# Kernel optimization log

Hardware: AMD Instinct MI355X
Metric: run time of the kernel (lower is better)

The kernel has to match this reference:

```python
import jax, jax.numpy as jnp
import numpy as np

N_HEADS = 8
N_DIM = 512
ATTN_DIM = N_DIM // N_HEADS
SOFT_TEMPERATURE = 1.0
TEMPERATURE = ATTN_DIM ** 0.5 / SOFT_TEMPERATURE


def sparsemax(z):
    # sparsemax along last axis: euclidean projection onto the simplex
    n = z.shape[-1]
    z_sorted = -jnp.sort(-z, axis=-1)                      # descending
    cs = jnp.cumsum(z_sorted, axis=-1)
    k = jnp.arange(1, n + 1, dtype=z.dtype)
    support = 1.0 + k * z_sorted > cs                      # bool
    k_sel = jnp.sum(support, axis=-1, keepdims=True)       # support size >= 1
    cs_sel = jnp.take_along_axis(cs, k_sel - 1, axis=-1)
    tau = (cs_sel - 1.0) / k_sel.astype(z.dtype)
    return jnp.maximum(z - tau, 0.0)


def setup_inputs() -> dict:
    key = jax.random.key(0)
    ks = jax.random.split(key, 9)
    bs, L, d = 8, 1024, N_DIM
    s = 1.0 / np.sqrt(d)
    return {
        "h_q": jax.random.normal(ks[0], (bs, L, d), jnp.float32),
        "h_k": jax.random.normal(ks[1], (bs, L, d), jnp.float32),
        "h_v": jax.random.normal(ks[2], (bs, L, d), jnp.float32),
        "Wq": jax.random.normal(ks[3], (d, d), jnp.float32) * s,
        "Wk": jax.random.normal(ks[4], (d, d), jnp.float32) * s,
        "Wv": jax.random.normal(ks[5], (d, d), jnp.float32) * s,
        "bv": jax.random.normal(ks[6], (d,), jnp.float32) * s,
        "Wf": jax.random.normal(ks[7], (d, d), jnp.float32) * s,
        "bf": jax.random.normal(ks[8], (d,), jnp.float32) * s,
    }


def reference(h_q, h_k, h_v, Wq, Wk, Wv, bv, Wf, bf):
    bs, Lq, _ = h_q.shape
    Lk = h_k.shape[1]
    H, D = N_HEADS, ATTN_DIM
    q = (h_q @ Wq.T).reshape(bs, Lq, H, D).transpose(0, 2, 1, 3)   # bhqd
    k = (h_k @ Wk.T).reshape(bs, Lk, H, D).transpose(0, 2, 1, 3)   # bhkd
    v = (h_v @ Wv.T + bv).reshape(bs, Lk, H, D).transpose(0, 2, 1, 3)
    alpha = jnp.einsum('bhqd,bhkd->bhqk', q / TEMPERATURE, k)
    alpha = sparsemax(alpha)
    res = jnp.einsum('bhqk,bhkd->bhqd', alpha, v)
    res = res.transpose(0, 2, 1, 3).reshape(bs, Lq, H * D)
    return res @ Wf.T + bf
```

## Files before the change

kernel.cpp:

```cpp
#include <hip/hip_runtime.h>
#include <hip/hip_bf16.h>
#include <cstdint>
#include <cstddef>

#define BS 8
#define SEQ 1024
#define DMODEL 512
#define NHEADS 8
#define DHEAD 64
#define QBLK 16
#define PPAD 1032

typedef float f32x4 __attribute__((ext_vector_type(4)));
typedef short bf16x8 __attribute__((ext_vector_type(8)));

static __device__ __forceinline__ unsigned short f2bf(float v) {
    __hip_bfloat16 hb = __float2bfloat16(v);
    return *reinterpret_cast<unsigned short*>(&hb);
}

struct CvtJob { const float* s; unsigned short* d; int n4; };

__global__ __launch_bounds__(256) void cvt_many(
    CvtJob j0, CvtJob j1, CvtJob j2, CvtJob j3, CvtJob j4, CvtJob j5, CvtJob j6)
{
    CvtJob j;
    switch (blockIdx.y) {
        case 0: j = j0; break; case 1: j = j1; break; case 2: j = j2; break;
        case 3: j = j3; break; case 4: j = j4; break; case 5: j = j5; break;
        default: j = j6; break;
    }
    for (int i = blockIdx.x * 256 + threadIdx.x; i < j.n4; i += gridDim.x * 256) {
        const float4 f = ((const float4*)j.s)[i];
        uint2 u;
        u.x = (unsigned)f2bf(f.x) | ((unsigned)f2bf(f.y) << 16);
        u.y = (unsigned)f2bf(f.z) | ((unsigned)f2bf(f.w) << 16);
        ((uint2*)j.d)[i] = u;
    }
}

struct GArgs { const unsigned short* A; const unsigned short* W;
               const float* bias; void* C; float scale; int mode; };

__global__ __launch_bounds__(256) void gemm_mfma(GArgs g0, GArgs g1, GArgs g2) {
    __shared__ __align__(16) unsigned short As[64 * 64];
    __shared__ __align__(16) unsigned short Bs[128 * 64];

    const GArgs g = (blockIdx.z == 0) ? g0 : ((blockIdx.z == 1) ? g1 : g2);
    const int tid = threadIdx.x;
    const int w = tid >> 6, l = tid & 63, lr = l & 15, lg = l >> 4;
    const int bm = blockIdx.y * 64, bn = blockIdx.x * 128;
    const int mrow = (w & 1) * 32, ncol = (w >> 1) * 64;

    f32x4 acc[2][4];
#pragma unroll
    for (int mt = 0; mt < 2; ++mt)
#pragma unroll
        for (int nt = 0; nt < 4; ++nt) acc[mt][nt] = (f32x4)0.f;

    for (int k0 = 0; k0 < DMODEL; k0 += 64) {
#pragma unroll
        for (int i = 0; i < 2; ++i) {
            const int rbase = i * 32 + w * 8;
            const int r = rbase + (l >> 3);
            const unsigned short* src = g.A + (size_t)(bm + r) * DMODEL + k0
                                        + 8 * ((l & 7) ^ (r & 7));
            __builtin_amdgcn_global_load_lds((const unsigned int*)src,
                                             (unsigned int*)&As[rbase * 64], 16, 0, 0);
        }
#pragma unroll
        for (int i = 0; i < 4; ++i) {
            const int rbase = i * 32 + w * 8;
            const int r = rbase + (l >> 3);
            const unsigned short* src = g.W + (size_t)(bn + r) * DMODEL + k0
                                        + 8 * ((l & 7) ^ (r & 7));
            __builtin_amdgcn_global_load_lds((const unsigned int*)src,
                                             (unsigned int*)&Bs[rbase * 64], 16, 0, 0);
        }
        __syncthreads();
#pragma unroll
        for (int kk = 0; kk < 2; ++kk) {
            bf16x8 av[2], bv[4];
#pragma unroll
            for (int mt = 0; mt < 2; ++mt) {
                const int ra = mrow + mt * 16 + lr;
                av[mt] = *(const bf16x8*)&As[ra * 64 + 8 * ((kk * 4 + lg) ^ (ra & 7))];
            }
#pragma unroll
            for (int nt = 0; nt < 4; ++nt) {
                const int rb = ncol + nt * 16 + lr;
                bv[nt] = *(const bf16x8*)&Bs[rb * 64 + 8 * ((kk * 4 + lg) ^ (rb & 7))];
            }
#pragma unroll
            for (int mt = 0; mt < 2; ++mt)
#pragma unroll
                for (int nt = 0; nt < 4; ++nt)
                    acc[mt][nt] = __builtin_amdgcn_mfma_f32_16x16x32_bf16(
                        av[mt], bv[nt], acc[mt][nt], 0, 0, 0);
        }
        __syncthreads();
    }

    if (g.mode == 0) {
        float* C = (float*)g.C;
#pragma unroll
        for (int mt = 0; mt < 2; ++mt)
#pragma unroll
        for (int nt = 0; nt < 4; ++nt)
#pragma unroll
        for (int j = 0; j < 4; ++j) {
            const int r = bm + mrow + mt * 16 + lg * 4 + j;
            const int c = bn + ncol + nt * 16 + lr;
            C[(size_t)r * DMODEL + c] = acc[mt][nt][j] * g.scale
                                        + (g.bias ? g.bias[c] : 0.f);
        }
    } else if (g.mode == 1) {
        unsigned short* C = (unsigned short*)g.C;
#pragma unroll
        for (int mt = 0; mt < 2; ++mt)
#pragma unroll
        for (int nt = 0; nt < 4; ++nt)
#pragma unroll
        for (int j = 0; j < 4; ++j) {
            const int r = bm + mrow + mt * 16 + lg * 4 + j;
            const int c = bn + ncol + nt * 16 + lr;
            const float v = acc[mt][nt][j] * g.scale + (g.bias ? g.bias[c] : 0.f);
            const int b = r >> 10, ll = r & (SEQ - 1);
            const int h = c >> 6, dd = c & 63;
            C[((size_t)(b * NHEADS + h) * SEQ + ll) * DHEAD + dd] = f2bf(v);
        }
    } else {
        unsigned short* C = (unsigned short*)g.C;
#pragma unroll
        for (int mt = 0; mt < 2; ++mt)
#pragma unroll
        for (int nt = 0; nt < 4; ++nt) {
            const int c = bn + ncol + nt * 16 + lr;
            const int h = c >> 6, dd = c & 63;
            const int r0 = bm + mrow + mt * 16 + lg * 4;
            const int b = r0 >> 10, l0 = r0 & (SEQ - 1);
            unsigned short tmp[4];
#pragma unroll
            for (int j = 0; j < 4; ++j)
                tmp[j] = f2bf(acc[mt][nt][j] * g.scale + (g.bias ? g.bias[c] : 0.f));
            uint2 u;
            u.x = (unsigned)tmp[0] | ((unsigned)tmp[1] << 16);
            u.y = (unsigned)tmp[2] | ((unsigned)tmp[3] << 16);
            *(uint2*)&C[((size_t)(b * NHEADS + h) * DHEAD + dd) * SEQ + l0] = u;
        }
    }
}

__global__ __launch_bounds__(256, 4) void attn_mfma(
    const unsigned short* __restrict__ Q, const unsigned short* __restrict__ K,
    const unsigned short* __restrict__ Vt, unsigned short* __restrict__ R)
{
    __shared__ __align__(16) unsigned short P[QBLK][PPAD];
    __shared__ __align__(16) float clist[QBLK][68];
    __shared__ int cnt_s[QBLK];
    __shared__ __align__(16) float red_m[QBLK][4];
    __shared__ __align__(16) float red_s[2][QBLK][4];
    __shared__ __align__(16) float red_c[2][QBLK][4];

    const int tid = threadIdx.x;
    const int w = tid >> 6, l = tid & 63, lr = l & 15, lg = l >> 4;

    const int flat = blockIdx.x;
    const int nid = (flat & 7) * 512 + (flat >> 3);
    const int q0 = (nid & 63) * QBLK;
    const int h = (nid >> 6) & (NHEADS - 1);
    const int b = nid >> 9;

    const size_t base = (size_t)(b * NHEADS + h) * SEQ * DHEAD;
    const unsigned short* Qp = Q + base;
    const unsigned short* Kp = K + base;

    const int ks = w * 256;

    const bf16x8 aq0 = *(const bf16x8*)(Qp + (size_t)(q0 + lr) * DHEAD + lg * 8);
    const bf16x8 aq1 = *(const bf16x8*)(Qp + (size_t)(q0 + lr) * DHEAD + 32 + lg * 8);
#define KROW(T) (Kp + (size_t)(ks + (T) * 16 + lr) * DHEAD + lg * 8)
    bf16x8 ka0 = *(const bf16x8*)KROW(0), kb0 = *(const bf16x8*)(KROW(0) + 32);
    bf16x8 ka1 = *(const bf16x8*)KROW(1), kb1 = *(const bf16x8*)(KROW(1) + 32);
    bf16x8 ka2 = *(const bf16x8*)KROW(2), kb2 = *(const bf16x8*)(KROW(2) + 32);
    bf16x8 ka3 = *(const bf16x8*)KROW(3), kb3 = *(const bf16x8*)(KROW(3) + 32);
    f32x4 acc[16];
#pragma unroll
    for (int t = 0; t < 16; ++t) acc[t] = (f32x4)0.f;
#define QK_STEP(T, KA, KB)                                                     \
    {                                                                          \
        acc[T] = __builtin_amdgcn_mfma_f32_16x16x32_bf16(KA, aq0, acc[T], 0, 0, 0); \
        acc[T] = __builtin_amdgcn_mfma_f32_16x16x32_bf16(KB, aq1, acc[T], 0, 0, 0); \
        if ((T) + 4 < 16) {                                                    \
            KA = *(const bf16x8*)KROW((T) + 4);                                \
            KB = *(const bf16x8*)(KROW((T) + 4) + 32);                         \
        }                                                                      \
    }
#pragma unroll
    for (int t = 0; t < 16; t += 4) {
        QK_STEP(t + 0, ka0, kb0)
        QK_STEP(t + 1, ka1, kb1)
        QK_STEP(t + 2, ka2, kb2)
        QK_STEP(t + 3, ka3, kb3)
    }
#undef QK_STEP
#undef KROW

    f32x4 m4 = acc[0];
#pragma unroll
    for (int t = 1; t < 16; ++t) {
        m4[0] = fmaxf(m4[0], acc[t][0]); m4[1] = fmaxf(m4[1], acc[t][1]);
        m4[2] = fmaxf(m4[2], acc[t][2]); m4[3] = fmaxf(m4[3], acc[t][3]);
    }
    float m = fmaxf(fmaxf(m4[0], m4[1]), fmaxf(m4[2], m4[3]));
    m = fmaxf(m, __shfl_xor(m, 16));
    m = fmaxf(m, __shfl_xor(m, 32));
    if (lg == 0) red_m[lr][w] = m;

    for (int i = tid; i < QBLK * 68; i += 256) (&clist[0][0])[i] = -3.0e38f;
    if (tid < QBLK) cnt_s[tid] = 0;
    __syncthreads();

    const float4 rm4 = *(const float4*)red_m[lr];
    const float rmax = fmaxf(fmaxf(rm4.x, rm4.y), fmaxf(rm4.z, rm4.w));
    float tau = rmax - 1.0f;
    const float thr = tau;

#pragma unroll
    for (int t = 0; t < 16; ++t)
#pragma unroll
        for (int j = 0; j < 4; ++j) {
            const float z = acc[t][j];
            if (z > thr) {
                const int pos = atomicAdd(&cnt_s[lr], 1);
                if (pos < 64) clist[lr][pos] = z;
            }
        }
    __syncthreads();

    const bool anyfull = __any(cnt_s[lr] > 64);

    if (!anyfull) {
        const f32x4* clp = (const f32x4*)&clist[lr][lg * 16];
        const f32x4 cd0 = clp[0], cd1 = clp[1], cd2 = clp[2], cd3 = clp[3];
        for (int it = 0; it < 16; ++it) {
            float s = 0.f, c = 0.f;
#pragma unroll
            for (int i = 0; i < 4; ++i) {
                const float z0 = cd0[i], z1 = cd1[i], z2 = cd2[i], z3 = cd3[i];
                if (z0 > tau) { s += z0; c += 1.f; }
                if (z1 > tau) { s += z1; c += 1.f; }
                if (z2 > tau) { s += z2; c += 1.f; }
                if (z3 > tau) { s += z3; c += 1.f; }
            }
            s += __shfl_xor(s, 16); c += __shfl_xor(c, 16);
            s += __shfl_xor(s, 32); c += __shfl_xor(c, 32);
            const float tn = (s - 1.f) / c;
            float delta = tn - tau;
            tau = tn;
            delta = fmaxf(delta, __shfl_xor(delta, 1));
            delta = fmaxf(delta, __shfl_xor(delta, 2));
            delta = fmaxf(delta, __shfl_xor(delta, 4));
            delta = fmaxf(delta, __shfl_xor(delta, 8));
            if (delta < 1e-5f) break;
        }
    } else {
        for (int it = 0; it < 16; ++it) {
            const int bb = (it + 1) & 1;
            float s = 0.f, c = 0.f;
#pragma unroll
            for (int t = 0; t < 16; ++t)
#pragma unroll
                for (int j = 0; j < 4; ++j) {
                    const float z = acc[t][j];
                    if (z > tau) { s += z; c += 1.f; }
                }
            s += __shfl_xor(s, 16); c += __shfl_xor(c, 16);
            s += __shfl_xor(s, 32); c += __shfl_xor(c, 32);
            if (lg == 0) { red_s[bb][lr][w] = s; red_c[bb][lr][w] = c; }
            __syncthreads();
            const float4 s4 = *(const float4*)red_s[bb][lr];
            const float4 c4 = *(const float4*)red_c[bb][lr];
            const float st = (s4.x + s4.y) + (s4.z + s4.w);
            const float ct = (c4.x + c4.y) + (c4.z + c4.w);
            const float tn = (st - 1.f) / ct;
            float delta = tn - tau;
            tau = tn;
            delta = fmaxf(delta, __shfl_xor(delta, 1));
            delta = fmaxf(delta, __shfl_xor(delta, 2));
            delta = fmaxf(delta, __shfl_xor(delta, 4));
            delta = fmaxf(delta, __shfl_xor(delta, 8));
            if (delta < 1e-5f) break;
        }
    }

#pragma unroll
    for (int t = 0; t < 16; ++t)
#pragma unroll
        for (int jp = 0; jp < 2; ++jp) {
            const unsigned lo = f2bf(fmaxf(acc[t][2 * jp] - tau, 0.f));
            const unsigned hi = f2bf(fmaxf(acc[t][2 * jp + 1] - tau, 0.f));
            *(unsigned*)&P[lr][ks + t * 16 + lg * 4 + 2 * jp] = lo | (hi << 16);
        }
    __syncthreads();

    const int dcol = w * 16;
    const unsigned short* VtP = Vt + ((size_t)(b * NHEADS + h) * DHEAD + dcol + lr) * SEQ
                                + lg * 8;
    f32x4 o = (f32x4)0.f;
    bf16x8 vb0 = *(const bf16x8*)(VtP + 0 * 32);
    bf16x8 vb1 = *(const bf16x8*)(VtP + 1 * 32);
    bf16x8 vb2 = *(const bf16x8*)(VtP + 2 * 32);
    bf16x8 vb3 = *(const bf16x8*)(VtP + 3 * 32);
#define PV_STEP(KT, VREG)                                                      \
    {                                                                          \
        const bf16x8 pa = *(const bf16x8*)&P[lr][(KT) * 32 + lg * 8];          \
        __builtin_amdgcn_s_setprio(1);                                         \
        o = __builtin_amdgcn_mfma_f32_16x16x32_bf16(pa, VREG, o, 0, 0, 0);     \
        __builtin_amdgcn_s_setprio(0);                                         \
        if ((KT) + 4 < 32) VREG = *(const bf16x8*)(VtP + ((KT) + 4) * 32);     \
    }
    for (int kt = 0; kt < 32; kt += 4) {
        PV_STEP(kt + 0, vb0)
        PV_STEP(kt + 1, vb1)
        PV_STEP(kt + 2, vb2)
        PV_STEP(kt + 3, vb3)
    }
#undef PV_STEP

#pragma unroll
    for (int j = 0; j < 4; ++j)
        R[((size_t)b * SEQ + q0 + lg * 4 + j) * DMODEL + h * DHEAD + dcol + lr] =
            f2bf(o[j]);
}

extern "C" void kernel_launch(void* const* d_in, const int* in_sizes, int n_in,
                              void* d_out, int out_size, void* d_ws, size_t ws_size,
                              hipStream_t stream) {
    const float* h_q = (const float*)d_in[0];
    const float* h_k = (const float*)d_in[1];
    const float* h_v = (const float*)d_in[2];
    const float* Wq  = (const float*)d_in[3];
    const float* Wk  = (const float*)d_in[4];
    const float* Wv  = (const float*)d_in[5];
    const float* bv  = (const float*)d_in[6];
    const float* Wf  = (const float*)d_in[7];
    const float* bf  = (const float*)d_in[8];
    float* out = (float*)d_out;

    const size_t perT = (size_t)BS * SEQ * DMODEL;
    const size_t wN = (size_t)DMODEL * DMODEL;
    unsigned short* hq_b = (unsigned short*)d_ws;
    unsigned short* hk_b = hq_b + perT;
    unsigned short* hv_b = hk_b + perT;
    unsigned short* Qws  = hv_b + perT;
    unsigned short* Kws  = Qws + perT;
    unsigned short* Vtw  = Kws + perT;
    unsigned short* Rws  = Vtw + perT;
    unsigned short* Wqb  = Rws + perT;
    unsigned short* Wkb  = Wqb + wN;
    unsigned short* Wvb  = Wkb + wN;
    unsigned short* Wfb  = Wvb + wN;

    {
        CvtJob j0{h_q, hq_b, (int)(perT / 4)};
        CvtJob j1{h_k, hk_b, (int)(perT / 4)};
        CvtJob j2{h_v, hv_b, (int)(perT / 4)};
        CvtJob j3{Wq, Wqb, (int)(wN / 4)};
        CvtJob j4{Wk, Wkb, (int)(wN / 4)};
        CvtJob j5{Wv, Wvb, (int)(wN / 4)};
        CvtJob j6{Wf, Wfb, (int)(wN / 4)};
        cvt_many<<<dim3(512, 7), 256, 0, stream>>>(j0, j1, j2, j3, j4, j5, j6);
    }

    {
        GArgs gq{hq_b, Wqb, nullptr, Qws, 0.125f, 1};
        GArgs gk{hk_b, Wkb, nullptr, Kws, 1.0f, 1};
        GArgs gv{hv_b, Wvb, bv,      Vtw, 1.0f, 2};
        gemm_mfma<<<dim3(DMODEL / 128, BS * SEQ / 64, 3), 256, 0, stream>>>(gq, gk, gv);
    }

    attn_mfma<<<dim3(BS * NHEADS * (SEQ / QBLK)), 256, 0, stream>>>(Qws, Kws, Vtw, Rws);

    {
        GArgs gf{Rws, Wfb, bf, out, 1.0f, 0};
        gemm_mfma<<<dim3(DMODEL / 128, BS * SEQ / 64, 1), 256, 0, stream>>>(gf, gf, gf);
    }
}
```

Before: 192.8 us.

## Compute sparse PV product by gathering V rows for sparsemax support only

Alongside each candidate score, the kernel now stores that score's key index. In the common path where every row's support fits in 64 candidates, the full P matrix write and the dense PV MFMA loop are skipped. Instead each thread gathers the selected V rows from a new row-major V copy and accumulates weighted sums directly. The V projection GEMM writes both transposed and row-major layouts, which adds global writes and workspace. The s_setprio hints around the PV MFMA are also removed.

New measurement: 190.6 us. No clear change (-1.2%).

```diff
diff --git a/kernel.cpp b/kernel.cpp
--- a/kernel.cpp
+++ b/kernel.cpp
@@ -40,7 +40,7 @@
 }
 
 struct GArgs { const unsigned short* A; const unsigned short* W;
-               const float* bias; void* C; float scale; int mode; };
+               const float* bias; void* C; void* C2; float scale; int mode; };
 
 __global__ __launch_bounds__(256) void gemm_mfma(GArgs g0, GArgs g1, GArgs g2) {
     __shared__ __align__(16) unsigned short As[64 * 64];
@@ -114,53 +114,59 @@
             C[(size_t)r * DMODEL + c] = acc[mt][nt][j] * g.scale
                                         + (g.bias ? g.bias[c] : 0.f);
         }
-    } else if (g.mode == 1) {
-        unsigned short* C = (unsigned short*)g.C;
-#pragma unroll
-        for (int mt = 0; mt < 2; ++mt)
-#pragma unroll
-        for (int nt = 0; nt < 4; ++nt)
-#pragma unroll
-        for (int j = 0; j < 4; ++j) {
-            const int r = bm + mrow + mt * 16 + lg * 4 + j;
-            const int c = bn + ncol + nt * 16 + lr;
-            const float v = acc[mt][nt][j] * g.scale + (g.bias ? g.bias[c] : 0.f);
-            const int b = r >> 10, ll = r & (SEQ - 1);
-            const int h = c >> 6, dd = c & 63;
-            C[((size_t)(b * NHEADS + h) * SEQ + ll) * DHEAD + dd] = f2bf(v);
-        }
     } else {
-        unsigned short* C = (unsigned short*)g.C;
-#pragma unroll
-        for (int mt = 0; mt < 2; ++mt)
-#pragma unroll
-        for (int nt = 0; nt < 4; ++nt) {
-            const int c = bn + ncol + nt * 16 + lr;
-            const int h = c >> 6, dd = c & 63;
-            const int r0 = bm + mrow + mt * 16 + lg * 4;
-            const int b = r0 >> 10, l0 = r0 & (SEQ - 1);
-            unsigned short tmp[4];
-#pragma unroll
-            for (int j = 0; j < 4; ++j)
-                tmp[j] = f2bf(acc[mt][nt][j] * g.scale + (g.bias ? g.bias[c] : 0.f));
-            uint2 u;
-            u.x = (unsigned)tmp[0] | ((unsigned)tmp[1] << 16);
-            u.y = (unsigned)tmp[2] | ((unsigned)tmp[3] << 16);
-            *(uint2*)&C[((size_t)(b * NHEADS + h) * DHEAD + dd) * SEQ + l0] = u;
+        if (g.mode == 1 || g.mode == 3) {
+            unsigned short* C = (unsigned short*)g.C;
+#pragma unroll
+            for (int mt = 0; mt < 2; ++mt)
+#pragma unroll
+            for (int nt = 0; nt < 4; ++nt)
+#pragma unroll
+            for (int j = 0; j < 4; ++j) {
+                const int r = bm + mrow + mt * 16 + lg * 4 + j;
+                const int c = bn + ncol + nt * 16 + lr;
+                const float v = acc[mt][nt][j] * g.scale + (g.bias ? g.bias[c] : 0.f);
+                const int b = r >> 10, ll = r & (SEQ - 1);
+                const int h = c >> 6, dd = c & 63;
+                C[((size_t)(b * NHEADS + h) * SEQ + ll) * DHEAD + dd] = f2bf(v);
+            }
+        }
+        if (g.mode == 2 || g.mode == 3) {
+            unsigned short* C = (unsigned short*)((g.mode == 3) ? g.C2 : g.C);
+#pragma unroll
+            for (int mt = 0; mt < 2; ++mt)
+#pragma unroll
+            for (int nt = 0; nt < 4; ++nt) {
+                const int c = bn + ncol + nt * 16 + lr;
+                const int h = c >> 6, dd = c & 63;
+                const int r0 = bm + mrow + mt * 16 + lg * 4;
+                const int b = r0 >> 10, l0 = r0 & (SEQ - 1);
+                unsigned short tmp[4];
+#pragma unroll
+                for (int j = 0; j < 4; ++j)
+                    tmp[j] = f2bf(acc[mt][nt][j] * g.scale + (g.bias ? g.bias[c] : 0.f));
+                uint2 u;
+                u.x = (unsigned)tmp[0] | ((unsigned)tmp[1] << 16);
+                u.y = (unsigned)tmp[2] | ((unsigned)tmp[3] << 16);
+                *(uint2*)&C[((size_t)(b * NHEADS + h) * DHEAD + dd) * SEQ + l0] = u;
+            }
         }
     }
 }
 
 __global__ __launch_bounds__(256, 4) void attn_mfma(
     const unsigned short* __restrict__ Q, const unsigned short* __restrict__ K,
-    const unsigned short* __restrict__ Vt, unsigned short* __restrict__ R)
+    const unsigned short* __restrict__ Vt, const unsigned short* __restrict__ Vn,
+    unsigned short* __restrict__ R)
 {
     __shared__ __align__(16) unsigned short P[QBLK][PPAD];
-    __shared__ __align__(16) float clist[QBLK][68];
+    __shared__ __align__(16) float clist[QBLK][66];
+    __shared__ __align__(16) unsigned short cidx[QBLK][66];
     __shared__ int cnt_s[QBLK];
     __shared__ __align__(16) float red_m[QBLK][4];
     __shared__ __align__(16) float red_s[2][QBLK][4];
     __shared__ __align__(16) float red_c[2][QBLK][4];
+    __shared__ float tau_s[QBLK];
 
     const int tid = threadIdx.x;
     const int w = tid >> 6, l = tid & 63, lr = l & 15, lg = l >> 4;
@@ -217,7 +223,7 @@
     m = fmaxf(m, __shfl_xor(m, 32));
     if (lg == 0) red_m[lr][w] = m;
 
-    for (int i = tid; i < QBLK * 68; i += 256) (&clist[0][0])[i] = -3.0e38f;
+    for (int i = tid; i < QBLK * 66; i += 256) (&clist[0][0])[i] = -3.0e38f;
     if (tid < QBLK) cnt_s[tid] = 0;
     __syncthreads();
 
@@ -233,7 +239,10 @@
             const float z = acc[t][j];
             if (z > thr) {
                 const int pos = atomicAdd(&cnt_s[lr], 1);
-                if (pos < 64) clist[lr][pos] = z;
+                if (pos < 64) {
+                    clist[lr][pos] = z;
+                    cidx[lr][pos] = (unsigned short)(ks + t * 16 + lg * 4 + j);
+                }
             }
         }
     __syncthreads();
@@ -264,34 +273,78 @@
             delta = fmaxf(delta, __shfl_xor(delta, 8));
             if (delta < 1e-5f) break;
         }
-    } else {
-        for (int it = 0; it < 16; ++it) {
-            const int bb = (it + 1) & 1;
-            float s = 0.f, c = 0.f;
-#pragma unroll
-            for (int t = 0; t < 16; ++t)
-#pragma unroll
-                for (int j = 0; j < 4; ++j) {
-                    const float z = acc[t][j];
-                    if (z > tau) { s += z; c += 1.f; }
-                }
-            s += __shfl_xor(s, 16); c += __shfl_xor(c, 16);
-            s += __shfl_xor(s, 32); c += __shfl_xor(c, 32);
-            if (lg == 0) { red_s[bb][lr][w] = s; red_c[bb][lr][w] = c; }
-            __syncthreads();
-            const float4 s4 = *(const float4*)red_s[bb][lr];
-            const float4 c4 = *(const float4*)red_c[bb][lr];
-            const float st = (s4.x + s4.y) + (s4.z + s4.w);
-            const float ct = (c4.x + c4.y) + (c4.z + c4.w);
-            const float tn = (st - 1.f) / ct;
-            float delta = tn - tau;
-            tau = tn;
-            delta = fmaxf(delta, __shfl_xor(delta, 1));
-            delta = fmaxf(delta, __shfl_xor(delta, 2));
-            delta = fmaxf(delta, __shfl_xor(delta, 4));
-            delta = fmaxf(delta, __shfl_xor(delta, 8));
-            if (delta < 1e-5f) break;
-        }
+        if (w == 0 && lg == 0) tau_s[lr] = tau;
+        __syncthreads();
+
+        const int r = tid >> 4;
+        const int dt = tid & 15;
+        const float taur = tau_s[r];
+        const int cntc = cnt_s[r];
+        const unsigned short* Vrow = Vn + base + dt * 4;
+        f32x4 o = (f32x4)0.f;
+        float z0, z1, z2, z3;
+        uint2 v0, v1, v2, v3;
+#define SLOAD(ZS, VS, I)                                                       \
+    {                                                                          \
+        const int ii = (I) < cntc ? (I) : 0;                                   \
+        ZS = clist[r][ii];                                                     \
+        VS = *(const uint2*)(Vrow + (size_t)cidx[r][ii] * DHEAD);              \
+    }
+#define SMAC(ZS, VS)                                                           \
+    {                                                                          \
+        const float wgt = fmaxf(ZS - taur, 0.f);                               \
+        o[0] += wgt * __uint_as_float(VS.x << 16);                             \
+        o[1] += wgt * __uint_as_float(VS.x & 0xffff0000u);                     \
+        o[2] += wgt * __uint_as_float(VS.y << 16);                             \
+        o[3] += wgt * __uint_as_float(VS.y & 0xffff0000u);                     \
+    }
+        SLOAD(z0, v0, 0) SLOAD(z1, v1, 1) SLOAD(z2, v2, 2) SLOAD(z3, v3, 3)
+        for (int i = 0; i < cntc; i += 4) {
+            SMAC(z0, v0)
+            if (i + 1 < cntc) SMAC(z1, v1)
+            if (i + 2 < cntc) SMAC(z2, v2)
+            if (i + 3 < cntc) SMAC(z3, v3)
+            SLOAD(z0, v0, i + 4) SLOAD(z1, v1, i + 5)
+            SLOAD(z2, v2, i + 6) SLOAD(z3, v3, i + 7)
+        }
+#undef SLOAD
+#undef SMAC
+        unsigned short t4[4];
+#pragma unroll
+        for (int j = 0; j < 4; ++j) t4[j] = f2bf(o[j]);
+        uint2 u;
+        u.x = (unsigned)t4[0] | ((unsigned)t4[1] << 16);
+        u.y = (unsigned)t4[2] | ((unsigned)t4[3] << 16);
+        *(uint2*)&R[((size_t)b * SEQ + q0 + r) * DMODEL + h * DHEAD + dt * 4] = u;
+        return;
+    }
+
+    for (int it = 0; it < 16; ++it) {
+        const int bb = (it + 1) & 1;
+        float s = 0.f, c = 0.f;
+#pragma unroll
+        for (int t = 0; t < 16; ++t)
+#pragma unroll
+            for (int j = 0; j < 4; ++j) {
+                const float z = acc[t][j];
+                if (z > tau) { s += z; c += 1.f; }
+            }
+        s += __shfl_xor(s, 16); c += __shfl_xor(c, 16);
+        s += __shfl_xor(s, 32); c += __shfl_xor(c, 32);
+        if (lg == 0) { red_s[bb][lr][w] = s; red_c[bb][lr][w] = c; }
+        __syncthreads();
+        const float4 s4 = *(const float4*)red_s[bb][lr];
+        const float4 c4 = *(const float4*)red_c[bb][lr];
+        const float st = (s4.x + s4.y) + (s4.z + s4.w);
+        const float ct = (c4.x + c4.y) + (c4.z + c4.w);
+        const float tn = (st - 1.f) / ct;
+        float delta = tn - tau;
+        tau = tn;
+        delta = fmaxf(delta, __shfl_xor(delta, 1));
+        delta = fmaxf(delta, __shfl_xor(delta, 2));
+        delta = fmaxf(delta, __shfl_xor(delta, 4));
+        delta = fmaxf(delta, __shfl_xor(delta, 8));
+        if (delta < 1e-5f) break;
     }
 
 #pragma unroll
@@ -315,9 +368,7 @@
 #define PV_STEP(KT, VREG)                                                      \
     {                                                                          \
         const bf16x8 pa = *(const bf16x8*)&P[lr][(KT) * 32 + lg * 8];          \
-        __builtin_amdgcn_s_setprio(1);                                         \
         o = __builtin_amdgcn_mfma_f32_16x16x32_bf16(pa, VREG, o, 0, 0, 0);     \
-        __builtin_amdgcn_s_setprio(0);                                         \
         if ((KT) + 4 < 32) VREG = *(const bf16x8*)(VtP + ((KT) + 4) * 32);     \
     }
     for (int kt = 0; kt < 32; kt += 4) {
@@ -356,7 +407,8 @@
     unsigned short* Qws  = hv_b + perT;
     unsigned short* Kws  = Qws + perT;
     unsigned short* Vtw  = Kws + perT;
-    unsigned short* Rws  = Vtw + perT;
+    unsigned short* Vnw  = Vtw + perT;
+    unsigned short* Rws  = Vnw + perT;
     unsigned short* Wqb  = Rws + perT;
     unsigned short* Wkb  = Wqb + wN;
     unsigned short* Wvb  = Wkb + wN;
@@ -374,16 +426,16 @@
     }
 
     {
-        GArgs gq{hq_b, Wqb, nullptr, Qws, 0.125f, 1};
-        GArgs gk{hk_b, Wkb, nullptr, Kws, 1.0f, 1};
-        GArgs gv{hv_b, Wvb, bv,      Vtw, 1.0f, 2};
+        GArgs gq{hq_b, Wqb, nullptr, Qws, nullptr, 0.125f, 1};
+        GArgs gk{hk_b, Wkb, nullptr, Kws, nullptr, 1.0f, 1};
+        GArgs gv{hv_b, Wvb, bv,      Vnw, Vtw,     1.0f, 3};
         gemm_mfma<<<dim3(DMODEL / 128, BS * SEQ / 64, 3), 256, 0, stream>>>(gq, gk, gv);
     }
 
-    attn_mfma<<<dim3(BS * NHEADS * (SEQ / QBLK)), 256, 0, stream>>>(Qws, Kws, Vtw, Rws);
+    attn_mfma<<<dim3(BS * NHEADS * (SEQ / QBLK)), 256, 0, stream>>>(Qws, Kws, Vtw, Vnw, Rws);
 
     {
-        GArgs gf{Rws, Wfb, bf, out, 1.0f, 0};
+        GArgs gf{Rws, Wfb, bf, out, nullptr, 1.0f, 0};
         gemm_mfma<<<dim3(DMODEL / 128, BS * SEQ / 64, 1), 256, 0, stream>>>(gf, gf, gf);
     }
 }
```
